# Kernel optimization log

Hardware: AMD Instinct MI355X
Metric: run time of the kernel (lower is better)

Reference implementation:

```python
import jax, jax.numpy as jnp
import numpy as np

K = 2  # top-k experts per token

def setup_inputs() -> dict:
    key = jax.random.key(0)
    ks = jax.random.split(key, 8)
    B, S, D, F, E = 2, 1024, 1024, 4096, 8
    s_in = 1.0 / np.sqrt(D)
    s_mid = 1.0 / np.sqrt(F)
    return {
        "x": jax.random.normal(ks[0], (B, S, D), dtype=jnp.float32),
        "Wr": jax.random.uniform(ks[1], (D, E), jnp.float32, -s_in, s_in),
        "br": jax.random.uniform(ks[2], (E,), jnp.float32, -s_in, s_in),
        "W1": jax.random.uniform(ks[3], (E, D, F), jnp.float32, -s_in, s_in),
        "b1": jax.random.uniform(ks[4], (E, F), jnp.float32, -s_in, s_in),
        "W2": jax.random.uniform(ks[5], (E, F, D), jnp.float32, -s_mid, s_mid),
        "b2": jax.random.uniform(ks[6], (E, D), jnp.float32, -s_mid, s_mid),
    }

def _moe(x, Wr, br, W1, b1, W2, b2):
    E = Wr.shape[1]
    # router (eval mode: no noise)
    logits = jnp.einsum('bsd,de->bse', x, Wr) + br          # [B,S,E]
    topk_logits, topk_idx = jax.lax.top_k(logits, K)        # [B,S,K]
    router_probs = jax.nn.softmax(topk_logits, axis=-1)     # [B,S,K]
    # per-expert combine weight: sum over k slots assigned to expert e
    onehot = jax.nn.one_hot(topk_idx, E, dtype=x.dtype)     # [B,S,K,E]
    w = jnp.einsum('bske,bsk->bse', onehot, router_probs)   # [B,S,E]
    # scan over experts (fixed small E), accumulate weighted expert outputs
    def step(acc, ew):
        W1j, b1j, W2j, b2j, wj = ew                          # wj: [B,S]
        h = jax.nn.gelu(jnp.einsum('bsd,df->bsf', x, W1j) + b1j, approximate=False)
        y = jnp.einsum('bsf,fd->bsd', h, W2j) + b2j
        return acc + y * wj[..., None], None
    out, _ = jax.lax.scan(step, jnp.zeros_like(x),
                          (W1, b1, W2, b2, jnp.transpose(w, (2, 0, 1))))
    return out, router_probs

def reference(x, Wr, br, W1, b1, W2, b2):
    return _moe(x, Wr, br, W1, b1, W2, b2)
```

## Files before the change

kernel.cpp:

```cpp
#include <hip/hip_runtime.h>
#include <hip/hip_bf16.h>
#include <cstdint>

#define TOKENS 2048
#define Dm 1024
#define Fm 4096
#define Em 8

typedef short s16x8 __attribute__((ext_vector_type(8)));
typedef float f32x4 __attribute__((ext_vector_type(4)));

#define GLOAD16(g, l) __builtin_amdgcn_global_load_lds(                     \
    (const __attribute__((address_space(1))) void*)(g),                     \
    (__attribute__((address_space(3))) void*)(l), 16, 0, 0)

__device__ __forceinline__ ushort f2bf(float f) {
  union { float f; uint32_t u; } v; v.f = f;
  uint32_t r = v.u + 0x7fffu + ((v.u >> 16) & 1u);
  return (ushort)(r >> 16);
}

__global__ void transcvt(const float* __restrict__ in, ushort* __restrict__ out,
                         int R, int C) {
  __shared__ float tile[32 * 33];
  int e = blockIdx.z;
  const float* src = in + (size_t)e * R * C;
  ushort* dst = out + (size_t)e * R * C;
  int c0 = blockIdx.x * 32, r0 = blockIdx.y * 32;
  int lr = threadIdx.x >> 5, lc = threadIdx.x & 31;
#pragma unroll
  for (int p = 0; p < 4; ++p)
    tile[(p * 8 + lr) * 33 + lc] = src[(size_t)(r0 + p * 8 + lr) * C + c0 + lc];
  __syncthreads();
#pragma unroll
  for (int p = 0; p < 4; ++p)
    dst[(size_t)(c0 + p * 8 + lr) * R + r0 + lc] = f2bf(tile[lc * 33 + p * 8 + lr]);
}

__global__ void prep(const float* __restrict__ W1, ushort* __restrict__ W1T,
                     const float* __restrict__ x, const float* __restrict__ Wr,
                     const float* __restrict__ br, float* __restrict__ probs,
                     int* __restrict__ e_sel, float* __restrict__ w_sel,
                     ushort* __restrict__ xb) {
  __shared__ float shf[32 * 33];
  int b = blockIdx.x;
  if (b < 32768) {
    int cx = b & 127, ry = (b >> 7) & 31, e = b >> 12;
    const float* src = W1 + ((size_t)e * Dm + ry * 32) * Fm + cx * 32;
    int lr = threadIdx.x >> 5, lc = threadIdx.x & 31;
#pragma unroll
    for (int p = 0; p < 4; ++p)
      shf[(p * 8 + lr) * 33 + lc] = src[(size_t)(p * 8 + lr) * Fm + lc];
    __syncthreads();
#pragma unroll
    for (int p = 0; p < 4; ++p)
      W1T[((size_t)e * Fm + cx * 32 + p * 8 + lr) * Dm + ry * 32 + lc] =
          f2bf(shf[lc * 33 + p * 8 + lr]);
    return;
  }
  int t = b - 32768;
  const float4* xr4 = (const float4*)(x + (size_t)t * Dm);
  float4 v = xr4[threadIdx.x];
  ushort4 o;
  o.x = f2bf(v.x); o.y = f2bf(v.y); o.z = f2bf(v.z); o.w = f2bf(v.w);
  ((ushort4*)(xb + (size_t)t * Dm))[threadIdx.x] = o;

  int d0 = threadIdx.x * 4;
  const float4* wr4 = (const float4*)(Wr + (size_t)d0 * Em);
  float wv[4][8];
#pragma unroll
  for (int r = 0; r < 4; ++r) {
    float4 a = wr4[r * 2], bq = wr4[r * 2 + 1];
    wv[r][0] = a.x; wv[r][1] = a.y; wv[r][2] = a.z; wv[r][3] = a.w;
    wv[r][4] = bq.x; wv[r][5] = bq.y; wv[r][6] = bq.z; wv[r][7] = bq.w;
  }
  float xs[4] = {v.x, v.y, v.z, v.w};
  float acc[Em];
#pragma unroll
  for (int e = 0; e < Em; ++e)
    acc[e] = xs[0] * wv[0][e] + xs[1] * wv[1][e] + xs[2] * wv[2][e] + xs[3] * wv[3][e];
#pragma unroll
  for (int off = 32; off >= 1; off >>= 1)
#pragma unroll
    for (int e = 0; e < Em; ++e) acc[e] += __shfl_down(acc[e], off);
  float* red = shf;
  int lane = threadIdx.x & 63, wid = threadIdx.x >> 6;
  if (lane == 0)
#pragma unroll
    for (int e = 0; e < Em; ++e) red[wid * 8 + e] = acc[e];
  __syncthreads();
  if (threadIdx.x == 0) {
    float lg[Em];
#pragma unroll
    for (int e = 0; e < Em; ++e)
      lg[e] = red[e] + red[8 + e] + red[16 + e] + red[24 + e] + br[e];
    int i0 = 0;
    for (int e = 1; e < Em; ++e) if (lg[e] > lg[i0]) i0 = e;
    int i1 = -1;
    for (int e = 0; e < Em; ++e) {
      if (e == i0) continue;
      if (i1 < 0 || lg[e] > lg[i1]) i1 = e;
    }
    float d = lg[i1] - lg[i0];
    float tt = expf(d);
    float inv = 1.f / (1.f + tt);
    probs[t * 2] = inv; probs[t * 2 + 1] = tt * inv;
    e_sel[t * 2] = i0; e_sel[t * 2 + 1] = i1;
    w_sel[t * 2] = inv; w_sel[t * 2 + 1] = tt * inv;
  }
}

__global__ void build2(const int* __restrict__ e_sel, const float* __restrict__ w_sel,
                       int* __restrict__ tok_of_row, float* __restrict__ w_of_row,
                       int* __restrict__ base, int* __restrict__ npad,
                       const float* __restrict__ b2, float* __restrict__ out) {
  int tid = threadIdx.x;
  if (blockIdx.x != 0) {
    int t = blockIdx.x - 1;
    int e0 = e_sel[2 * t], e1 = e_sel[2 * t + 1];
    float w0 = w_sel[2 * t], w1 = w_sel[2 * t + 1];
    const float4* p0 = (const float4*)(b2 + (size_t)e0 * Dm);
    const float4* p1 = (const float4*)(b2 + (size_t)e1 * Dm);
    float4* o = (float4*)(out + (size_t)t * Dm);
    float4 a = p0[tid], b = p1[tid];
    float4 r;
    r.x = w0 * a.x + w1 * b.x; r.y = w0 * a.y + w1 * b.y;
    r.z = w0 * a.z + w1 * b.z; r.w = w0 * a.w + w1 * b.w;
    o[tid] = r;
    return;
  }
  __shared__ int cnt[Em], run[Em], sbase[Em];
  __shared__ int wsum[4][Em];
  int lane = tid & 63, wid = tid >> 6;
  if (tid < Em) { cnt[tid] = 0; run[tid] = 0; }
  __syncthreads();
  for (int t = tid; t < TOKENS; t += 256) {
    atomicAdd(&cnt[e_sel[2 * t]], 1);
    atomicAdd(&cnt[e_sel[2 * t + 1]], 1);
  }
  __syncthreads();
  if (tid == 0) {
    int b = 0;
    for (int e = 0; e < Em; ++e) {
      base[e] = b; sbase[e] = b;
      int n = cnt[e];
      int p = (n + 127) & ~127;
      npad[e] = p; b += p;
    }
  }
  __syncthreads();
  for (int c = 0; c < TOKENS / 256; ++c) {
    int t = c * 256 + tid;
    int e0 = e_sel[2 * t], e1 = e_sel[2 * t + 1];
    unsigned long long mm[Em];
#pragma unroll
    for (int e = 0; e < Em; ++e) {
      unsigned long long m0 = __ballot(e0 == e);
      unsigned long long m1 = __ballot(e1 == e);
      mm[e] = m0 | m1;
      if (lane == 0) wsum[wid][e] = __popcll(mm[e]);
    }
    __syncthreads();
    unsigned long long below = (1ull << lane) - 1ull;
    {
      int e = e0;
      int p = __popcll(mm[e] & below);
      int pre = 0;
      for (int w = 0; w < wid; ++w) pre += wsum[w][e];
      int row = sbase[e] + run[e] + pre + p;
      tok_of_row[row] = t; w_of_row[row] = w_sel[2 * t];
    }
    {
      int e = e1;
      int p = __popcll(mm[e] & below);
      int pre = 0;
      for (int w = 0; w < wid; ++w) pre += wsum[w][e];
      int row = sbase[e] + run[e] + pre + p;
      tok_of_row[row] = t; w_of_row[row] = w_sel[2 * t + 1];
    }
    __syncthreads();
    if (tid < Em) {
      int s = 0;
      for (int w = 0; w < 4; ++w) s += wsum[w][tid];
      run[tid] += s;
    }
    __syncthreads();
  }
  for (int e = 0; e < Em; ++e) {
    int n = cnt[e];
    int p = (n + 127) & ~127;
    for (int i = n + tid; i < p; i += 256) {
      tok_of_row[sbase[e] + i] = -1;
      w_of_row[sbase[e] + i] = 0.f;
    }
  }
}

__global__ __launch_bounds__(256) void gemm1(
    const ushort* __restrict__ xb, const ushort* __restrict__ W1T,
    const float* __restrict__ b1, ushort* __restrict__ H,
    const int* __restrict__ tok_of_row, const int* __restrict__ base,
    const int* __restrict__ npad,
    const float* __restrict__ W2, ushort* __restrict__ W2T, int do_w2) {
  __shared__ ushort sbuf[8192];
  __shared__ int toks[128];
  int tid = threadIdx.x, lane = tid & 63, wid = tid >> 6;
  int e = blockIdx.y >> 4, rt = blockIdx.y & 15;
  int nt = npad[e] >> 7;
  if (rt >= nt) {
    if (!do_w2) return;
    int act = 0, pre = 0;
#pragma unroll
    for (int e2 = 0; e2 < Em; ++e2) {
      int n2 = npad[e2] >> 7;
      act += n2;
      if (e2 < e) pre += 16 - n2;
    }
    int idle_id = (pre + rt - nt) * 32 + blockIdx.x;
    int total_idle = (128 - act) * 32;
    float* ft = (float*)sbuf;
    int lr = tid >> 5, lc = tid & 31;
    for (int t = idle_id; t < 32768; t += total_idle) {
      int x2 = t & 31, y2 = (t >> 5) & 127, e2 = t >> 12;
      const float* src = W2 + ((size_t)e2 * Fm + y2 * 32) * Dm + x2 * 32;
#pragma unroll
      for (int p = 0; p < 4; ++p)
        ft[(p * 8 + lr) * 33 + lc] = src[(size_t)(p * 8 + lr) * Dm + lc];
      __syncthreads();
#pragma unroll
      for (int p = 0; p < 4; ++p)
        W2T[((size_t)e2 * Dm + x2 * 32 + p * 8 + lr) * Fm + y2 * 32 + lc] =
            f2bf(ft[lc * 33 + p * 8 + lr]);
      __syncthreads();
    }
    return;
  }
  int row0 = base[e] + rt * 128;
  int n0 = blockIdx.x * 128;
  if (tid < 128) toks[tid] = tok_of_row[row0 + tid];
  __syncthreads();
  ushort* As = sbuf;
  ushort* Bs = sbuf + 4096;
  int arow = tid >> 2, asub = tid & 3;
  int sw = ((asub ^ ((arow >> 1) & 3)) << 3);
  int t0 = toks[arow];      if (t0 < 0) t0 = 0;
  int t1 = toks[64 + arow]; if (t1 < 0) t1 = 0;
  const ushort* sA0 = xb + (size_t)t0 * Dm + sw;
  const ushort* sA1 = xb + (size_t)t1 * Dm + sw;
  const ushort* sB0 = W1T + ((size_t)e * Fm + n0 + arow) * Dm + sw;
  const ushort* sB1 = sB0 + (size_t)64 * Dm;
  char* ldA0 = (char*)As + wid * 1024;
  char* ldA1 = (char*)As + 4096 + wid * 1024;
  char* ldB0 = (char*)Bs + wid * 1024;
  char* ldB1 = (char*)Bs + 4096 + wid * 1024;
  int wr2 = wid >> 1, wc2 = wid & 1;
  int g = lane >> 4, c = (lane >> 1) & 3;
  int aidx = (wr2 * 64 + (lane & 15)) * 32 + ((g ^ c) << 3);
  int bidx = (wc2 * 64 + (lane & 15)) * 32 + ((g ^ c) << 3);
  f32x4 acc[4][4] = {};
  for (int kt = 0; kt < Dm / 32; ++kt) {
    GLOAD16(sA0, ldA0);
    GLOAD16(sA1, ldA1);
    GLOAD16(sB0, ldB0);
    GLOAD16(sB1, ldB1);
    sA0 += 32; sA1 += 32; sB0 += 32; sB1 += 32;
    __syncthreads();
    s16x8 av[4], bv[4];
#pragma unroll
    for (int m = 0; m < 4; ++m) av[m] = *(const s16x8*)(As + aidx + m * 512);
#pragma unroll
    for (int n = 0; n < 4; ++n) bv[n] = *(const s16x8*)(Bs + bidx + n * 512);
#pragma unroll
    for (int m = 0; m < 4; ++m)
#pragma unroll
      for (int n = 0; n < 4; ++n)
        acc[m][n] = __builtin_amdgcn_mfma_f32_16x16x32_bf16(av[m], bv[n], acc[m][n], 0, 0, 0);
    __syncthreads();
  }
#pragma unroll
  for (int p = 0; p < 2; ++p) {
    if (wr2 == p) {
#pragma unroll
      for (int n = 0; n < 4; ++n) {
        int col = wc2 * 64 + (lane & 15) + n * 16;
        float bias = b1[e * Fm + n0 + col];
#pragma unroll
        for (int m = 0; m < 4; ++m) {
#pragma unroll
          for (int j = 0; j < 4; ++j) {
            float v = acc[m][n][j] + bias;
            float gl = 0.5f * v * (1.f + erff(v * 0.70710678118654752f));
            sbuf[(g * 4 + m * 16 + j) * 128 + col] = f2bf(gl);
          }
        }
      }
    }
    __syncthreads();
#pragma unroll
    for (int q = 0; q < 4; ++q) {
      int id = q * 256 + tid;
      int r = id >> 4, ch = id & 15;
      *(s16x8*)(H + (size_t)(row0 + p * 64 + r) * Fm + n0 + ch * 8) =
          *(const s16x8*)(sbuf + r * 128 + ch * 8);
    }
    __syncthreads();
  }
}

__global__ __launch_bounds__(256) void gemm2(
    const ushort* __restrict__ H, const ushort* __restrict__ W2T,
    const int* __restrict__ tok_of_row, const float* __restrict__ w_of_row,
    const int* __restrict__ base, const int* __restrict__ npad,
    float* __restrict__ out) {
  __shared__ ushort sbuf[8192];
  __shared__ int toks[128];
  __shared__ float wts[128];
  int tid = threadIdx.x, lane = tid & 63, wid = tid >> 6;
  int e = blockIdx.y >> 4, rt = blockIdx.y & 15;
  int nt = npad[e] >> 7;
  if (rt >= nt) return;
  int row0 = base[e] + rt * 128;
  int n0 = blockIdx.x * 128;
  int k0 = blockIdx.z * (Fm / 2);
  if (tid < 128) {
    toks[tid] = tok_of_row[row0 + tid];
    wts[tid] = w_of_row[row0 + tid];
  }
  __syncthreads();
  ushort* As = sbuf;
  ushort* Bs = sbuf + 4096;
  int arow = tid >> 2, asub = tid & 3;
  int sw = ((asub ^ ((arow >> 1) & 3)) << 3);
  const ushort* sA0 = H + (size_t)(row0 + arow) * Fm + k0 + sw;
  const ushort* sA1 = sA0 + (size_t)64 * Fm;
  const ushort* sB0 = W2T + ((size_t)e * Dm + n0 + arow) * Fm + k0 + sw;
  const ushort* sB1 = sB0 + (size_t)64 * Fm;
  char* ldA0 = (char*)As + wid * 1024;
  char* ldA1 = (char*)As + 4096 + wid * 1024;
  char* ldB0 = (char*)Bs + wid * 1024;
  char* ldB1 = (char*)Bs + 4096 + wid * 1024;
  int wr2 = wid >> 1, wc2 = wid & 1;
  int g = lane >> 4, c = (lane >> 1) & 3;
  int aidx = (wr2 * 64 + (lane & 15)) * 32 + ((g ^ c) << 3);
  int bidx = (wc2 * 64 + (lane & 15)) * 32 + ((g ^ c) << 3);
  f32x4 acc[4][4] = {};
  for (int kt = 0; kt < Fm / 2 / 32; ++kt) {
    GLOAD16(sA0, ldA0);
    GLOAD16(sA1, ldA1);
    GLOAD16(sB0, ldB0);
    GLOAD16(sB1, ldB1);
    sA0 += 32; sA1 += 32; sB0 += 32; sB1 += 32;
    __syncthreads();
    s16x8 av[4], bv[4];
#pragma unroll
    for (int m = 0; m < 4; ++m) av[m] = *(const s16x8*)(As + aidx + m * 512);
#pragma unroll
    for (int n = 0; n < 4; ++n) bv[n] = *(const s16x8*)(Bs + bidx + n * 512);
#pragma unroll
    for (int m = 0; m < 4; ++m)
#pragma unroll
      for (int n = 0; n < 4; ++n)
        acc[m][n] = __builtin_amdgcn_mfma_f32_16x16x32_bf16(av[m], bv[n], acc[m][n], 0, 0, 0);
    __syncthreads();
  }
  int rb = wr2 * 64 + g * 4;
  int cb = n0 + wc2 * 64 + (lane & 15);
#pragma unroll
  for (int n = 0; n < 4; ++n) {
    int col = cb + n * 16;
#pragma unroll
    for (int m = 0; m < 4; ++m) {
      int rl = rb + m * 16;
#pragma unroll
      for (int j = 0; j < 4; ++j) {
        int tok = toks[rl + j];
        if (tok >= 0)
          atomicAdd(&out[(size_t)tok * Dm + col], wts[rl + j] * acc[m][n][j]);
      }
    }
  }
}

extern "C" void kernel_launch(void* const* d_in, const int* in_sizes, int n_in,
                              void* d_out, int out_size, void* d_ws, size_t ws_size,
                              hipStream_t stream) {
  const float* x  = (const float*)d_in[0];
  const float* Wr = (const float*)d_in[1];
  const float* br = (const float*)d_in[2];
  const float* W1 = (const float*)d_in[3];
  const float* b1 = (const float*)d_in[4];
  const float* W2 = (const float*)d_in[5];
  const float* b2 = (const float*)d_in[6];
  float* out = (float*)d_out;
  float* probs = out + (size_t)TOKENS * Dm;

  char* ws = (char*)d_ws;
  ushort* W1T  = (ushort*)ws;
  ushort* Hbuf = (ushort*)(ws + 67108864);
  ushort* xb   = (ushort*)(ws + 109051904);
  int*   tok_of_row = (int*)(ws + 113246208);
  float* w_of_row   = (float*)(ws + 113266688);
  int*   e_sel      = (int*)(ws + 113287168);
  float* w_sel      = (float*)(ws + 113303552);
  int*   meta       = (int*)(ws + 113319936);
  int sep = (ws_size >= 180429056ULL) ? 1 : 0;
  ushort* W2T = sep ? (ushort*)(ws + 113320192) : W1T;

  prep<<<32768 + TOKENS, 256, 0, stream>>>(W1, W1T, x, Wr, br, probs, e_sel, w_sel, xb);
  build2<<<TOKENS + 1, 256, 0, stream>>>(e_sel, w_sel, tok_of_row, w_of_row,
                                         meta, meta + 8, b2, out);
  gemm1<<<dim3(32, 128), 256, 0, stream>>>(xb, W1T, b1, Hbuf, tok_of_row,
                                           meta, meta + 8, W2, W2T, sep);
  if (!sep)
    transcvt<<<dim3(Dm / 32, Fm / 32, Em), 256, 0, stream>>>(W2, W2T, Fm, Dm);
  gemm2<<<dim3(8, 128, 2), 256, 0, stream>>>(Hbuf, W2T, tok_of_row, w_of_row,
                                             meta, meta + 8, out);
}
```

Baseline: 303.8 us.

## Double-buffer LDS in both GEMMs and move W2 transpose into prep

New measurement: 325.9 us. 1.07x slower.

```diff
diff --git a/kernel.cpp b/kernel.cpp
--- a/kernel.cpp
+++ b/kernel.cpp
@@ -19,6 +19,30 @@
   uint32_t r = v.u + 0x7fffu + ((v.u >> 16) & 1u);
   return (ushort)(r >> 16);
 }
+
+__device__ __forceinline__ void kstep(const ushort* sbuf, int eoff, int aidx,
+                                      int bidx, f32x4 (&acc)[4][4]) {
+  s16x8 av[4], bv[4];
+#pragma unroll
+  for (int m = 0; m < 4; ++m)
+    av[m] = *(const s16x8*)(sbuf + eoff + aidx + m * 512);
+#pragma unroll
+  for (int n = 0; n < 4; ++n)
+    bv[n] = *(const s16x8*)(sbuf + eoff + 4096 + bidx + n * 512);
+#pragma unroll
+  for (int m = 0; m < 4; ++m)
+#pragma unroll
+    for (int n = 0; n < 4; ++n)
+      acc[m][n] = __builtin_amdgcn_mfma_f32_16x16x32_bf16(av[m], bv[n], acc[m][n], 0, 0, 0);
+}
+
+#define STAGE4(boff) {                                                      \
+    char* bb = (char*)sbuf + (boff);                                        \
+    GLOAD16(sA0, bb + wid * 1024);                                          \
+    GLOAD16(sA1, bb + 4096 + wid * 1024);                                   \
+    GLOAD16(sB0, bb + 8192 + wid * 1024);                                   \
+    GLOAD16(sB1, bb + 12288 + wid * 1024);                                  \
+    sA0 += 32; sA1 += 32; sB0 += 32; sB1 += 32; }
 
 __global__ void transcvt(const float* __restrict__ in, ushort* __restrict__ out,
                          int R, int C) {
@@ -38,27 +62,42 @@
 }
 
 __global__ void prep(const float* __restrict__ W1, ushort* __restrict__ W1T,
+                     const float* __restrict__ W2, ushort* __restrict__ W2T,
+                     int do_w2,
                      const float* __restrict__ x, const float* __restrict__ Wr,
                      const float* __restrict__ br, float* __restrict__ probs,
                      int* __restrict__ e_sel, float* __restrict__ w_sel,
                      ushort* __restrict__ xb) {
   __shared__ float shf[32 * 33];
   int b = blockIdx.x;
-  if (b < 32768) {
-    int cx = b & 127, ry = (b >> 7) & 31, e = b >> 12;
-    const float* src = W1 + ((size_t)e * Dm + ry * 32) * Fm + cx * 32;
+  if (b < 65536) {
+    const float* src;
+    ushort* dst;
+    size_t sstride, dstride;
+    if (b < 32768) {
+      int cx = b & 127, ry = (b >> 7) & 31, e = b >> 12;
+      src = W1 + ((size_t)e * Dm + ry * 32) * Fm + cx * 32;
+      dst = W1T + ((size_t)e * Fm + cx * 32) * Dm + ry * 32;
+      sstride = Fm; dstride = Dm;
+    } else {
+      if (!do_w2) return;
+      int b2i = b - 32768;
+      int cx = b2i & 31, ry = (b2i >> 5) & 127, e = b2i >> 12;
+      src = W2 + ((size_t)e * Fm + ry * 32) * Dm + cx * 32;
+      dst = W2T + ((size_t)e * Dm + cx * 32) * Fm + ry * 32;
+      sstride = Dm; dstride = Fm;
+    }
     int lr = threadIdx.x >> 5, lc = threadIdx.x & 31;
 #pragma unroll
     for (int p = 0; p < 4; ++p)
-      shf[(p * 8 + lr) * 33 + lc] = src[(size_t)(p * 8 + lr) * Fm + lc];
+      shf[(p * 8 + lr) * 33 + lc] = src[(size_t)(p * 8 + lr) * sstride + lc];
     __syncthreads();
 #pragma unroll
     for (int p = 0; p < 4; ++p)
-      W1T[((size_t)e * Fm + cx * 32 + p * 8 + lr) * Dm + ry * 32 + lc] =
-          f2bf(shf[lc * 33 + p * 8 + lr]);
+      dst[(size_t)(p * 8 + lr) * dstride + lc] = f2bf(shf[lc * 33 + p * 8 + lr]);
     return;
   }
-  int t = b - 32768;
+  int t = b - 65536;
   const float4* xr4 = (const float4*)(x + (size_t)t * Dm);
   float4 v = xr4[threadIdx.x];
   ushort4 o;
@@ -110,28 +149,12 @@
   }
 }
 
-__global__ void build2(const int* __restrict__ e_sel, const float* __restrict__ w_sel,
-                       int* __restrict__ tok_of_row, float* __restrict__ w_of_row,
-                       int* __restrict__ base, int* __restrict__ npad,
-                       const float* __restrict__ b2, float* __restrict__ out) {
-  int tid = threadIdx.x;
-  if (blockIdx.x != 0) {
-    int t = blockIdx.x - 1;
-    int e0 = e_sel[2 * t], e1 = e_sel[2 * t + 1];
-    float w0 = w_sel[2 * t], w1 = w_sel[2 * t + 1];
-    const float4* p0 = (const float4*)(b2 + (size_t)e0 * Dm);
-    const float4* p1 = (const float4*)(b2 + (size_t)e1 * Dm);
-    float4* o = (float4*)(out + (size_t)t * Dm);
-    float4 a = p0[tid], b = p1[tid];
-    float4 r;
-    r.x = w0 * a.x + w1 * b.x; r.y = w0 * a.y + w1 * b.y;
-    r.z = w0 * a.z + w1 * b.z; r.w = w0 * a.w + w1 * b.w;
-    o[tid] = r;
-    return;
-  }
+__global__ void build_lists(const int* __restrict__ e_sel, const float* __restrict__ w_sel,
+                            int* __restrict__ tok_of_row, float* __restrict__ w_of_row,
+                            int* __restrict__ base, int* __restrict__ npad) {
   __shared__ int cnt[Em], run[Em], sbase[Em];
   __shared__ int wsum[4][Em];
-  int lane = tid & 63, wid = tid >> 6;
+  int tid = threadIdx.x, lane = tid & 63, wid = tid >> 6;
   if (tid < Em) { cnt[tid] = 0; run[tid] = 0; }
   __syncthreads();
   for (int t = tid; t < TOKENS; t += 256) {
@@ -200,47 +223,17 @@
     const ushort* __restrict__ xb, const ushort* __restrict__ W1T,
     const float* __restrict__ b1, ushort* __restrict__ H,
     const int* __restrict__ tok_of_row, const int* __restrict__ base,
-    const int* __restrict__ npad,
-    const float* __restrict__ W2, ushort* __restrict__ W2T, int do_w2) {
-  __shared__ ushort sbuf[8192];
+    const int* __restrict__ npad) {
+  __shared__ ushort sbuf[16384];
   __shared__ int toks[128];
   int tid = threadIdx.x, lane = tid & 63, wid = tid >> 6;
   int e = blockIdx.y >> 4, rt = blockIdx.y & 15;
   int nt = npad[e] >> 7;
-  if (rt >= nt) {
-    if (!do_w2) return;
-    int act = 0, pre = 0;
-#pragma unroll
-    for (int e2 = 0; e2 < Em; ++e2) {
-      int n2 = npad[e2] >> 7;
-      act += n2;
-      if (e2 < e) pre += 16 - n2;
-    }
-    int idle_id = (pre + rt - nt) * 32 + blockIdx.x;
-    int total_idle = (128 - act) * 32;
-    float* ft = (float*)sbuf;
-    int lr = tid >> 5, lc = tid & 31;
-    for (int t = idle_id; t < 32768; t += total_idle) {
-      int x2 = t & 31, y2 = (t >> 5) & 127, e2 = t >> 12;
-      const float* src = W2 + ((size_t)e2 * Fm + y2 * 32) * Dm + x2 * 32;
-#pragma unroll
-      for (int p = 0; p < 4; ++p)
-        ft[(p * 8 + lr) * 33 + lc] = src[(size_t)(p * 8 + lr) * Dm + lc];
-      __syncthreads();
-#pragma unroll
-      for (int p = 0; p < 4; ++p)
-        W2T[((size_t)e2 * Dm + x2 * 32 + p * 8 + lr) * Fm + y2 * 32 + lc] =
-            f2bf(ft[lc * 33 + p * 8 + lr]);
-      __syncthreads();
-    }
-    return;
-  }
+  if (rt >= nt) return;
   int row0 = base[e] + rt * 128;
   int n0 = blockIdx.x * 128;
   if (tid < 128) toks[tid] = tok_of_row[row0 + tid];
   __syncthreads();
-  ushort* As = sbuf;
-  ushort* Bs = sbuf + 4096;
   int arow = tid >> 2, asub = tid & 3;
   int sw = ((asub ^ ((arow >> 1) & 3)) << 3);
   int t0 = toks[arow];      if (t0 < 0) t0 = 0;
@@ -249,34 +242,25 @@
   const ushort* sA1 = xb + (size_t)t1 * Dm + sw;
   const ushort* sB0 = W1T + ((size_t)e * Fm + n0 + arow) * Dm + sw;
   const ushort* sB1 = sB0 + (size_t)64 * Dm;
-  char* ldA0 = (char*)As + wid * 1024;
-  char* ldA1 = (char*)As + 4096 + wid * 1024;
-  char* ldB0 = (char*)Bs + wid * 1024;
-  char* ldB1 = (char*)Bs + 4096 + wid * 1024;
   int wr2 = wid >> 1, wc2 = wid & 1;
   int g = lane >> 4, c = (lane >> 1) & 3;
   int aidx = (wr2 * 64 + (lane & 15)) * 32 + ((g ^ c) << 3);
   int bidx = (wc2 * 64 + (lane & 15)) * 32 + ((g ^ c) << 3);
   f32x4 acc[4][4] = {};
-  for (int kt = 0; kt < Dm / 32; ++kt) {
-    GLOAD16(sA0, ldA0);
-    GLOAD16(sA1, ldA1);
-    GLOAD16(sB0, ldB0);
-    GLOAD16(sB1, ldB1);
-    sA0 += 32; sA1 += 32; sB0 += 32; sB1 += 32;
-    __syncthreads();
-    s16x8 av[4], bv[4];
-#pragma unroll
-    for (int m = 0; m < 4; ++m) av[m] = *(const s16x8*)(As + aidx + m * 512);
-#pragma unroll
-    for (int n = 0; n < 4; ++n) bv[n] = *(const s16x8*)(Bs + bidx + n * 512);
-#pragma unroll
-    for (int m = 0; m < 4; ++m)
-#pragma unroll
-      for (int n = 0; n < 4; ++n)
-        acc[m][n] = __builtin_amdgcn_mfma_f32_16x16x32_bf16(av[m], bv[n], acc[m][n], 0, 0, 0);
-    __syncthreads();
-  }
+  STAGE4(0)
+  __syncthreads();
+  for (int t = 0; t < 30; t += 2) {
+    STAGE4(16384)
+    kstep(sbuf, 0, aidx, bidx, acc);
+    __syncthreads();
+    STAGE4(0)
+    kstep(sbuf, 8192, aidx, bidx, acc);
+    __syncthreads();
+  }
+  STAGE4(16384)
+  kstep(sbuf, 0, aidx, bidx, acc);
+  __syncthreads();
+  kstep(sbuf, 8192, aidx, bidx, acc);
 #pragma unroll
   for (int p = 0; p < 2; ++p) {
     if (wr2 == p) {
@@ -309,10 +293,11 @@
 
 __global__ __launch_bounds__(256) void gemm2(
     const ushort* __restrict__ H, const ushort* __restrict__ W2T,
+    const float* __restrict__ b2,
     const int* __restrict__ tok_of_row, const float* __restrict__ w_of_row,
     const int* __restrict__ base, const int* __restrict__ npad,
     float* __restrict__ out) {
-  __shared__ ushort sbuf[8192];
+  __shared__ ushort sbuf[16384];
   __shared__ int toks[128];
   __shared__ float wts[128];
   int tid = threadIdx.x, lane = tid & 63, wid = tid >> 6;
@@ -327,47 +312,38 @@
     wts[tid] = w_of_row[row0 + tid];
   }
   __syncthreads();
-  ushort* As = sbuf;
-  ushort* Bs = sbuf + 4096;
   int arow = tid >> 2, asub = tid & 3;
   int sw = ((asub ^ ((arow >> 1) & 3)) << 3);
   const ushort* sA0 = H + (size_t)(row0 + arow) * Fm + k0 + sw;
   const ushort* sA1 = sA0 + (size_t)64 * Fm;
   const ushort* sB0 = W2T + ((size_t)e * Dm + n0 + arow) * Fm + k0 + sw;
   const ushort* sB1 = sB0 + (size_t)64 * Fm;
-  char* ldA0 = (char*)As + wid * 1024;
-  char* ldA1 = (char*)As + 4096 + wid * 1024;
-  char* ldB0 = (char*)Bs + wid * 1024;
-  char* ldB1 = (char*)Bs + 4096 + wid * 1024;
   int wr2 = wid >> 1, wc2 = wid & 1;
   int g = lane >> 4, c = (lane >> 1) & 3;
   int aidx = (wr2 * 64 + (lane & 15)) * 32 + ((g ^ c) << 3);
   int bidx = (wc2 * 64 + (lane & 15)) * 32 + ((g ^ c) << 3);
   f32x4 acc[4][4] = {};
-  for (int kt = 0; kt < Fm / 2 / 32; ++kt) {
-    GLOAD16(sA0, ldA0);
-    GLOAD16(sA1, ldA1);
-    GLOAD16(sB0, ldB0);
-    GLOAD16(sB1, ldB1);
-    sA0 += 32; sA1 += 32; sB0 += 32; sB1 += 32;
-    __syncthreads();
-    s16x8 av[4], bv[4];
-#pragma unroll
-    for (int m = 0; m < 4; ++m) av[m] = *(const s16x8*)(As + aidx + m * 512);
-#pragma unroll
-    for (int n = 0; n < 4; ++n) bv[n] = *(const s16x8*)(Bs + bidx + n * 512);
-#pragma unroll
-    for (int m = 0; m < 4; ++m)
-#pragma unroll
-      for (int n = 0; n < 4; ++n)
-        acc[m][n] = __builtin_amdgcn_mfma_f32_16x16x32_bf16(av[m], bv[n], acc[m][n], 0, 0, 0);
-    __syncthreads();
-  }
+  STAGE4(0)
+  __syncthreads();
+  for (int t = 0; t < 62; t += 2) {
+    STAGE4(16384)
+    kstep(sbuf, 0, aidx, bidx, acc);
+    __syncthreads();
+    STAGE4(0)
+    kstep(sbuf, 8192, aidx, bidx, acc);
+    __syncthreads();
+  }
+  STAGE4(16384)
+  kstep(sbuf, 0, aidx, bidx, acc);
+  __syncthreads();
+  kstep(sbuf, 8192, aidx, bidx, acc);
   int rb = wr2 * 64 + g * 4;
   int cb = n0 + wc2 * 64 + (lane & 15);
+  int add_bias = (blockIdx.z == 0);
 #pragma unroll
   for (int n = 0; n < 4; ++n) {
     int col = cb + n * 16;
+    float bias = add_bias ? b2[e * Dm + col] : 0.f;
 #pragma unroll
     for (int m = 0; m < 4; ++m) {
       int rl = rb + m * 16;
@@ -375,7 +351,7 @@
       for (int j = 0; j < 4; ++j) {
         int tok = toks[rl + j];
         if (tok >= 0)
-          atomicAdd(&out[(size_t)tok * Dm + col], wts[rl + j] * acc[m][n][j]);
+          atomicAdd(&out[(size_t)tok * Dm + col], wts[rl + j] * (acc[m][n][j] + bias));
       }
     }
   }
@@ -406,13 +382,15 @@
   int sep = (ws_size >= 180429056ULL) ? 1 : 0;
   ushort* W2T = sep ? (ushort*)(ws + 113320192) : W1T;
 
-  prep<<<32768 + TOKENS, 256, 0, stream>>>(W1, W1T, x, Wr, br, probs, e_sel, w_sel, xb);
-  build2<<<TOKENS + 1, 256, 0, stream>>>(e_sel, w_sel, tok_of_row, w_of_row,
-                                         meta, meta + 8, b2, out);
+  hipMemsetAsync(out, 0, (size_t)TOKENS * Dm * sizeof(float), stream);
+  prep<<<65536 + TOKENS, 256, 0, stream>>>(W1, W1T, W2, W2T, sep, x, Wr, br,
+                                           probs, e_sel, w_sel, xb);
+  build_lists<<<1, 256, 0, stream>>>(e_sel, w_sel, tok_of_row, w_of_row,
+                                     meta, meta + 8);
   gemm1<<<dim3(32, 128), 256, 0, stream>>>(xb, W1T, b1, Hbuf, tok_of_row,
-                                           meta, meta + 8, W2, W2T, sep);
+                                           meta, meta + 8);
   if (!sep)
     transcvt<<<dim3(Dm / 32, Fm / 32, Em), 256, 0, stream>>>(W2, W2T, Fm, Dm);
-  gemm2<<<dim3(8, 128, 2), 256, 0, stream>>>(Hbuf, W2T, tok_of_row, w_of_row,
+  gemm2<<<dim3(8, 128, 2), 256, 0, stream>>>(Hbuf, W2T, b2, tok_of_row, w_of_row,
                                              meta, meta + 8, out);
 }
```
